# Performance work log

Hardware: AMD Instinct MI355X
Metric: run time of the kernel (lower is better)

## Reference

```python
import jax, jax.numpy as jnp
import numpy as np

N_NODES = 100000
N_EDGES = 1000000
D = 64
OUT = 64
EPS = 1e-5


def setup_inputs() -> dict:
    key = jax.random.key(0)
    k1, k2, k3, k4 = jax.random.split(key, 4)
    x = jax.random.normal(k1, (N_NODES, D), dtype=jnp.float32)
    edge_index = jax.random.randint(k2, (2, N_EDGES), 0, N_NODES, dtype=jnp.int64)
    # Linear(2*D, OUT): torch default init ~ U(-1/sqrt(fan_in), 1/sqrt(fan_in))
    bound = 1.0 / np.sqrt(2 * D)
    W = jax.random.uniform(k3, (2 * D, OUT), minval=-bound, maxval=bound, dtype=jnp.float32)
    b = jax.random.uniform(k4, (OUT,), minval=-bound, maxval=bound, dtype=jnp.float32)
    gamma = jnp.ones((OUT,), dtype=jnp.float32)
    beta = jnp.zeros((OUT,), dtype=jnp.float32)
    return {"x": x, "edge_index": edge_index, "W": W, "b": b, "gamma": gamma, "beta": beta}


def reference(x, edge_index, W, b, gamma, beta):
    row, col = edge_index[0], edge_index[1]
    # gather source features and scatter-add into destination nodes
    neighbor_sum = jax.ops.segment_sum(x[row], col, num_segments=x.shape[0])  # [N, D]
    h = jnp.concatenate([x, neighbor_sum], axis=-1)  # [N, 2D]
    h = h @ W + b  # [N, OUT]
    # LayerNorm over last dim
    mu = jnp.mean(h, axis=-1, keepdims=True)
    var = jnp.var(h, axis=-1, keepdims=True)
    h = (h - mu) * jax.lax.rsqrt(var + EPS) * gamma + beta
    return h
```

## Files before the change

### kernel.cpp

```cpp
#include <hip/hip_runtime.h>

#define NN 100000
#define NE 1000000
#define OUT_D 64
#define EPS 1e-5f

#define NB 196
#define COLS 512
#define BSTRIDE 6016
#define EPB 4096
#define NBLK1 245
#define NPROJ 1024

#define QCOLS 128
#define QCAP 2560

typedef __attribute__((ext_vector_type(8))) short bf16x8;
typedef __attribute__((ext_vector_type(4))) float f32x4;
typedef __attribute__((ext_vector_type(4))) int i32x4;

static __device__ __forceinline__ unsigned short f2bf(float f) {
    unsigned u = __float_as_uint(f);
    u += 0x7FFFu + ((u >> 16) & 1u);
    return (unsigned short)(u >> 16);
}
static __device__ __forceinline__ float bf2f(unsigned short s) {
    return __uint_as_float((unsigned)s << 16);
}

__global__ __launch_bounds__(256) void mega_kernel(
    const float* __restrict__ x, const float* __restrict__ W,
    const int* __restrict__ ei, int* __restrict__ gcur, unsigned* __restrict__ gbuf,
    unsigned short* __restrict__ y1, unsigned short* __restrict__ y2)
{
    const int tid = threadIdx.x;
    const int lane = tid & 63;
    const int wv = tid >> 6;

    if (blockIdx.x < NBLK1) {
        __shared__ int lcnt[NB];
        __shared__ int loff[NB + 1];
        __shared__ int lbase[NB];
        __shared__ int lcur[NB];
        __shared__ int wpart[4];
        __shared__ unsigned lbuf[EPB];
        __shared__ unsigned char lbkt[EPB];
        const int e0 = blockIdx.x * EPB;

        int rows[16], cols[16];
        #pragma unroll
        for (int j = 0; j < 16; ++j) {
            const int e = e0 + j * 256 + tid;
            const bool v = e < NE;
            rows[j] = v ? ei[e] : 0;
            cols[j] = v ? ei[NE + e] : -1;
        }
        for (int i = tid; i < NB; i += 256) lcnt[i] = 0;
        __syncthreads();
        #pragma unroll
        for (int j = 0; j < 16; ++j)
            if (cols[j] >= 0) atomicAdd(&lcnt[cols[j] >> 9], 1);
        __syncthreads();
        {
            const int c = (tid < NB) ? lcnt[tid] : 0;
            int s = c;
            #pragma unroll
            for (int o = 1; o < 64; o <<= 1) { int t = __shfl_up(s, o); if (lane >= o) s += t; }
            if (lane == 63) wpart[wv] = s;
            __syncthreads();
            int woff = 0;
            for (int ww = 0; ww < wv; ++ww) woff += wpart[ww];
            if (tid < NB) {
                loff[tid] = woff + s - c;
                lcur[tid] = woff + s - c;
                lbase[tid] = atomicAdd(&gcur[tid], c);
            }
            if (tid == NB - 1) loff[NB] = woff + s;
        }
        __syncthreads();
        #pragma unroll
        for (int j = 0; j < 16; ++j) {
            if (cols[j] >= 0) {
                const int b = cols[j] >> 9;
                const int p = atomicAdd(&lcur[b], 1);
                lbuf[p] = ((unsigned)rows[j] << 9) | (unsigned)(cols[j] & (COLS - 1));
                lbkt[p] = (unsigned char)b;
            }
        }
        __syncthreads();
        const int total = loff[NB];
        for (int t = tid; t < total; t += 256) {
            const int b = lbkt[t];
            const unsigned idx = (unsigned)(lbase[b] + (t - loff[b]));
            if (idx < BSTRIDE) gbuf[(size_t)b * BSTRIDE + idx] = lbuf[t];
        }
    } else {
        if (blockIdx.x == NBLK1 && tid < OUT_D)
            y2[(size_t)NN * OUT_D + tid] = 0;
        const int m = lane & 15;
        const int quad = lane >> 4;
        bf16x8 Wf[8][2];
        #pragma unroll
        for (int t = 0; t < 8; ++t)
            #pragma unroll
            for (int q = 0; q < 2; ++q) {
                bf16x8 f;
                #pragma unroll
                for (int j = 0; j < 8; ++j) {
                    const int k = q * 32 + quad * 8 + j;
                    const int krow = (t < 4) ? k : (64 + k);
                    const int col = (t & 3) * 16 + m;
                    f[j] = (short)f2bf(W[krow * 64 + col]);
                }
                Wf[t][q] = f;
            }
        for (int tile = (blockIdx.x - NBLK1) * 4 + wv; tile < NN / 16; tile += NPROJ * 4) {
            const int n0 = tile * 16;
            bf16x8 Af[2];
            #pragma unroll
            for (int q = 0; q < 2; ++q) {
                const float* px = x + (size_t)(n0 + m) * 64 + q * 32 + quad * 8;
                const f32x4 a0 = *(const f32x4*)px;
                const f32x4 a1 = *(const f32x4*)(px + 4);
                bf16x8 f;
                #pragma unroll
                for (int j = 0; j < 4; ++j) { f[j] = (short)f2bf(a0[j]); f[4 + j] = (short)f2bf(a1[j]); }
                Af[q] = f;
            }
            #pragma unroll
            for (int t = 0; t < 8; ++t) {
                f32x4 acc = {0.f, 0.f, 0.f, 0.f};
                acc = __builtin_amdgcn_mfma_f32_16x16x32_bf16(Af[0], Wf[t][0], acc, 0, 0, 0);
                acc = __builtin_amdgcn_mfma_f32_16x16x32_bf16(Af[1], Wf[t][1], acc, 0, 0, 0);
                unsigned short* __restrict__ dst = (t < 4) ? y1 : y2;
                const int colb = (t & 3) * 16 + m;
                #pragma unroll
                for (int r = 0; r < 4; ++r)
                    dst[(size_t)(n0 + quad * 4 + r) * 64 + colb] = f2bf(acc[r]);
            }
        }
    }
}

__global__ __launch_bounds__(256) void agg_kernel(
    const int* __restrict__ gcur, const unsigned* __restrict__ gbuf,
    const unsigned short* __restrict__ y1, const unsigned short* __restrict__ y2,
    const float* __restrict__ bias, const float* __restrict__ gamma,
    const float* __restrict__ beta, float* __restrict__ out)
{
    __shared__ int cofs[QCOLS + 1];
    __shared__ int ccur[QCOLS];
    __shared__ int ccnt[QCOLS];
    __shared__ int ldst[QCAP];
    const int tid = threadIdx.x;
    const int lane = tid & 63;
    const int wv = tid >> 6;
    const int b = blockIdx.x >> 2;
    const int q = blockIdx.x & 3;

    const int cntE = min(gcur[b], BSTRIDE);
    const unsigned* __restrict__ gb = gbuf + (size_t)b * BSTRIDE;

    for (int i = tid; i < QCOLS; i += 256) ccnt[i] = 0;
    for (int i = tid; i < QCAP; i += 256) ldst[i] = NN;
    __syncthreads();
    for (int i = tid; i < cntE; i += 256) {
        const unsigned p = gb[i];
        const unsigned c9 = p & 511u;
        if ((int)(c9 >> 7) == q) atomicAdd(&ccnt[c9 & (QCOLS - 1)], 1);
    }
    __syncthreads();
    if (tid < 64) {
        int v0 = (ccnt[2 * tid] + 3) & ~3;
        int v1 = (ccnt[2 * tid + 1] + 3) & ~3;
        const int tsum = v0 + v1;
        int s = tsum;
        #pragma unroll
        for (int o = 1; o < 64; o <<= 1) { int t = __shfl_up(s, o); if (tid >= o) s += t; }
        int run = s - tsum;
        cofs[2 * tid] = run;     ccur[2 * tid] = run;     run += v0;
        cofs[2 * tid + 1] = run; ccur[2 * tid + 1] = run; run += v1;
        if (tid == 63) cofs[QCOLS] = run;
    }
    __syncthreads();
    for (int i = tid; i < cntE; i += 256) {
        const unsigned p = gb[i];
        const unsigned c9 = p & 511u;
        if ((int)(c9 >> 7) == q) {
            const int pos = atomicAdd(&ccur[c9 & (QCOLS - 1)], 1);
            if (pos < QCAP) ldst[pos] = (int)(p >> 9);
        }
    }
    __syncthreads();

    const int n0 = (b << 9) + (q << 7);
    for (int cl = wv; cl < QCOLS; cl += 4) {
        const int n = n0 + cl;
        if (n >= NN) continue;
        const int st = min(cofs[cl], QCAP);
        const int en = min(cofs[cl + 1], QCAP);
        const int cnt = en - st;
        const int* __restrict__ cp = ldst + st;

        float acc = bf2f(y1[(size_t)n * OUT_D + lane]) + bias[lane];
        int i = 0;
        for (; i + 8 <= cnt; i += 8) {
            const i32x4 c0 = *(const i32x4*)(cp + i);
            const i32x4 c1 = *(const i32x4*)(cp + i + 4);
            const float v0 = bf2f(y2[(size_t)c0[0] * OUT_D + lane]);
            const float v1 = bf2f(y2[(size_t)c0[1] * OUT_D + lane]);
            const float v2 = bf2f(y2[(size_t)c0[2] * OUT_D + lane]);
            const float v3 = bf2f(y2[(size_t)c0[3] * OUT_D + lane]);
            const float v4 = bf2f(y2[(size_t)c1[0] * OUT_D + lane]);
            const float v5 = bf2f(y2[(size_t)c1[1] * OUT_D + lane]);
            const float v6 = bf2f(y2[(size_t)c1[2] * OUT_D + lane]);
            const float v7 = bf2f(y2[(size_t)c1[3] * OUT_D + lane]);
            acc += ((v0 + v1) + (v2 + v3)) + ((v4 + v5) + (v6 + v7));
        }
        if (i < cnt) {
            const i32x4 c0 = *(const i32x4*)(cp + i);
            const float v0 = bf2f(y2[(size_t)c0[0] * OUT_D + lane]);
            const float v1 = bf2f(y2[(size_t)c0[1] * OUT_D + lane]);
            const float v2 = bf2f(y2[(size_t)c0[2] * OUT_D + lane]);
            const float v3 = bf2f(y2[(size_t)c0[3] * OUT_D + lane]);
            acc += (v0 + v1) + (v2 + v3);
        }

        float sv = acc, sq = acc * acc;
        #pragma unroll
        for (int off = 32; off; off >>= 1) { sv += __shfl_xor(sv, off); sq += __shfl_xor(sq, off); }
        const float mu  = sv * (1.0f / OUT_D);
        const float var = sq * (1.0f / OUT_D) - mu * mu;
        const float inv = rsqrtf(var + EPS);
        out[(size_t)n * OUT_D + lane] = (acc - mu) * inv * gamma[lane] + beta[lane];
    }
}

extern "C" void kernel_launch(void* const* d_in, const int* in_sizes, int n_in,
                              void* d_out, int out_size, void* d_ws, size_t ws_size,
                              hipStream_t stream) {
    const float* x     = (const float*)d_in[0];
    const int*   ei    = (const int*)  d_in[1];
    const float* W     = (const float*)d_in[2];
    const float* b     = (const float*)d_in[3];
    const float* gamma = (const float*)d_in[4];
    const float* beta  = (const float*)d_in[5];
    float* out = (float*)d_out;

    char* p = (char*)d_ws;
    int*            gcur    = (int*)p;             p += 1024;
    unsigned*       gbuf    = (unsigned*)p;        p += (size_t)NB * BSTRIDE * 4;
    unsigned short* y1      = (unsigned short*)p;  p += (size_t)NN * OUT_D * 2;
    unsigned short* y2      = (unsigned short*)p;

    hipMemsetAsync(gcur, 0, NB * sizeof(int), stream);
    mega_kernel<<<NBLK1 + NPROJ, 256, 0, stream>>>(x, W, ei, gcur, gbuf, y1, y2);
    agg_kernel <<<NB * 4,        256, 0, stream>>>(gcur, gbuf, y1, y2, b, gamma, beta, out);
}
```

Measured before the change: 163.6 us.

## Interleave four destination nodes per wave in aggregation and use 512-thread blocks

Each wave in the aggregation kernel now gathers neighbor rows for four destination nodes at once, over a shared number of rounds of eight. This puts up to 32 independent y2 loads in flight per iteration, to hide gather latency better than walking one node at a time. Blocks grow to 512 threads (8 waves, 16 columns each), per-column padding is raised to multiples of 8, and the local edge buffer is enlarged to fit the extra padding. In exchange, every node in a group of four runs as many rounds as its highest-degree member, with padded slots reading a dummy row. That adds redundant loads and uses more registers per thread.

```diff
diff --git a/kernel.cpp b/kernel.cpp
--- a/kernel.cpp
+++ b/kernel.cpp
@@ -13,7 +13,7 @@
 #define NPROJ 1024
 
 #define QCOLS 128
-#define QCAP 2560
+#define QCAP 3072
 
 typedef __attribute__((ext_vector_type(8))) short bf16x8;
 typedef __attribute__((ext_vector_type(4))) float f32x4;
@@ -142,7 +142,7 @@
     }
 }
 
-__global__ __launch_bounds__(256) void agg_kernel(
+__global__ __launch_bounds__(512) void agg_kernel(
     const int* __restrict__ gcur, const unsigned* __restrict__ gbuf,
     const unsigned short* __restrict__ y1, const unsigned short* __restrict__ y2,
     const float* __restrict__ bias, const float* __restrict__ gamma,
@@ -161,18 +161,18 @@
     const int cntE = min(gcur[b], BSTRIDE);
     const unsigned* __restrict__ gb = gbuf + (size_t)b * BSTRIDE;
 
-    for (int i = tid; i < QCOLS; i += 256) ccnt[i] = 0;
-    for (int i = tid; i < QCAP; i += 256) ldst[i] = NN;
-    __syncthreads();
-    for (int i = tid; i < cntE; i += 256) {
+    for (int i = tid; i < QCOLS; i += 512) ccnt[i] = 0;
+    for (int i = tid; i < QCAP; i += 512) ldst[i] = NN;
+    __syncthreads();
+    for (int i = tid; i < cntE; i += 512) {
         const unsigned p = gb[i];
         const unsigned c9 = p & 511u;
         if ((int)(c9 >> 7) == q) atomicAdd(&ccnt[c9 & (QCOLS - 1)], 1);
     }
     __syncthreads();
     if (tid < 64) {
-        int v0 = (ccnt[2 * tid] + 3) & ~3;
-        int v1 = (ccnt[2 * tid + 1] + 3) & ~3;
+        int v0 = (ccnt[2 * tid] + 7) & ~7;
+        int v1 = (ccnt[2 * tid + 1] + 7) & ~7;
         const int tsum = v0 + v1;
         int s = tsum;
         #pragma unroll
@@ -183,7 +183,7 @@
         if (tid == 63) cofs[QCOLS] = run;
     }
     __syncthreads();
-    for (int i = tid; i < cntE; i += 256) {
+    for (int i = tid; i < cntE; i += 512) {
         const unsigned p = gb[i];
         const unsigned c9 = p & 511u;
         if ((int)(c9 >> 7) == q) {
@@ -194,45 +194,68 @@
     __syncthreads();
 
     const int n0 = (b << 9) + (q << 7);
-    for (int cl = wv; cl < QCOLS; cl += 4) {
-        const int n = n0 + cl;
-        if (n >= NN) continue;
-        const int st = min(cofs[cl], QCAP);
-        const int en = min(cofs[cl + 1], QCAP);
-        const int cnt = en - st;
-        const int* __restrict__ cp = ldst + st;
-
-        float acc = bf2f(y1[(size_t)n * OUT_D + lane]) + bias[lane];
-        int i = 0;
-        for (; i + 8 <= cnt; i += 8) {
-            const i32x4 c0 = *(const i32x4*)(cp + i);
-            const i32x4 c1 = *(const i32x4*)(cp + i + 4);
-            const float v0 = bf2f(y2[(size_t)c0[0] * OUT_D + lane]);
-            const float v1 = bf2f(y2[(size_t)c0[1] * OUT_D + lane]);
-            const float v2 = bf2f(y2[(size_t)c0[2] * OUT_D + lane]);
-            const float v3 = bf2f(y2[(size_t)c0[3] * OUT_D + lane]);
-            const float v4 = bf2f(y2[(size_t)c1[0] * OUT_D + lane]);
-            const float v5 = bf2f(y2[(size_t)c1[1] * OUT_D + lane]);
-            const float v6 = bf2f(y2[(size_t)c1[2] * OUT_D + lane]);
-            const float v7 = bf2f(y2[(size_t)c1[3] * OUT_D + lane]);
-            acc += ((v0 + v1) + (v2 + v3)) + ((v4 + v5) + (v6 + v7));
-        }
-        if (i < cnt) {
-            const i32x4 c0 = *(const i32x4*)(cp + i);
-            const float v0 = bf2f(y2[(size_t)c0[0] * OUT_D + lane]);
-            const float v1 = bf2f(y2[(size_t)c0[1] * OUT_D + lane]);
-            const float v2 = bf2f(y2[(size_t)c0[2] * OUT_D + lane]);
-            const float v3 = bf2f(y2[(size_t)c0[3] * OUT_D + lane]);
-            acc += (v0 + v1) + (v2 + v3);
-        }
-
-        float sv = acc, sq = acc * acc;
-        #pragma unroll
-        for (int off = 32; off; off >>= 1) { sv += __shfl_xor(sv, off); sq += __shfl_xor(sq, off); }
-        const float mu  = sv * (1.0f / OUT_D);
-        const float var = sq * (1.0f / OUT_D) - mu * mu;
-        const float inv = rsqrtf(var + EPS);
-        out[(size_t)n * OUT_D + lane] = (acc - mu) * inv * gamma[lane] + beta[lane];
+    #pragma unroll 1
+    for (int g = 0; g < 4; ++g) {
+        const int cl0 = wv * 16 + g * 4;
+        float acc[4];
+        int st4[4], cnt4[4];
+        #pragma unroll
+        for (int k = 0; k < 4; ++k) {
+            const int n = n0 + cl0 + k;
+            const int st = min(cofs[cl0 + k], QCAP);
+            const int en = min(cofs[cl0 + k + 1], QCAP);
+            st4[k] = st;
+            cnt4[k] = en - st;
+            acc[k] = (n < NN) ? (bf2f(y1[(size_t)n * OUT_D + lane]) + bias[lane]) : 0.f;
+        }
+        const int rounds = max(max(cnt4[0], cnt4[1]), max(cnt4[2], cnt4[3])) >> 3;
+        for (int r = 0; r < rounds; ++r) {
+            const int off = r << 3;
+            i32x4 ra[4], rb[4];
+            #pragma unroll
+            for (int k = 0; k < 4; ++k) {
+                const int po = min(st4[k] + off, QCAP - 8);
+                ra[k] = *(const i32x4*)(ldst + po);
+                rb[k] = *(const i32x4*)(ldst + po + 4);
+            }
+            #pragma unroll
+            for (int k = 0; k < 4; ++k) {
+                const bool act = off < cnt4[k];
+                #pragma unroll
+                for (int j = 0; j < 4; ++j) {
+                    ra[k][j] = act ? ra[k][j] : NN;
+                    rb[k][j] = act ? rb[k][j] : NN;
+                }
+            }
+            float v[4][8];
+            #pragma unroll
+            for (int k = 0; k < 4; ++k) {
+                v[k][0] = bf2f(y2[(size_t)ra[k][0] * OUT_D + lane]);
+                v[k][1] = bf2f(y2[(size_t)ra[k][1] * OUT_D + lane]);
+                v[k][2] = bf2f(y2[(size_t)ra[k][2] * OUT_D + lane]);
+                v[k][3] = bf2f(y2[(size_t)ra[k][3] * OUT_D + lane]);
+                v[k][4] = bf2f(y2[(size_t)rb[k][0] * OUT_D + lane]);
+                v[k][5] = bf2f(y2[(size_t)rb[k][1] * OUT_D + lane]);
+                v[k][6] = bf2f(y2[(size_t)rb[k][2] * OUT_D + lane]);
+                v[k][7] = bf2f(y2[(size_t)rb[k][3] * OUT_D + lane]);
+            }
+            #pragma unroll
+            for (int k = 0; k < 4; ++k)
+                acc[k] += ((v[k][0] + v[k][1]) + (v[k][2] + v[k][3])) +
+                          ((v[k][4] + v[k][5]) + (v[k][6] + v[k][7]));
+        }
+        #pragma unroll
+        for (int k = 0; k < 4; ++k) {
+            const int n = n0 + cl0 + k;
+            if (n >= NN) continue;
+            float sv = acc[k], sq = acc[k] * acc[k];
+            #pragma unroll
+            for (int off = 32; off; off >>= 1) { sv += __shfl_xor(sv, off); sq += __shfl_xor(sq, off); }
+            const float mu  = sv * (1.0f / OUT_D);
+            const float var = sq * (1.0f / OUT_D) - mu * mu;
+            const float inv = rsqrtf(var + EPS);
+            out[(size_t)n * OUT_D + lane] = (acc[k] - mu) * inv * gamma[lane] + beta[lane];
+        }
     }
 }
 
@@ -255,5 +278,5 @@
 
     hipMemsetAsync(gcur, 0, NB * sizeof(int), stream);
     mega_kernel<<<NBLK1 + NPROJ, 256, 0, stream>>>(x, W, ei, gcur, gbuf, y1, y2);
-    agg_kernel <<<NB * 4,        256, 0, stream>>>(gcur, gbuf, y1, y2, b, gamma, beta, out);
-}
+    agg_kernel <<<NB * 4,        512, 0, stream>>>(gcur, gbuf, y1, y2, b, gamma, beta, out);
+}
```

Measured after the change: 166.4 us. No clear change (+1.7%).

## Split aggregation into CSR placement and per-node output kernels; stage W via LDS

Applied to the files above, without the earlier changes.

The old aggregation kernel had only 784 blocks, each building a local CSR and then looping over 128 nodes. It is now split into two kernels. A place kernel writes the per-quarter CSR and a packed offset/length word per node to global memory. An out kernel then launches one wavefront per node (25000 blocks) for the gather, sum and layernorm, which gives much more parallelism to hide the latency of the random gathers. Separately, the mega kernel now converts W to bf16 into LDS once per block, transposed, instead of doing scalar global loads per fragment, and its shared memory is unioned into one buffer. The cost is an extra launch plus a global round trip for the CSR, and per-quarter capacity drops from 2560 to 2016 entries, which raises the risk of truncating high-degree buckets.

```diff
diff --git a/kernel.cpp b/kernel.cpp
--- a/kernel.cpp
+++ b/kernel.cpp
@@ -8,12 +8,15 @@
 #define NB 196
 #define COLS 512
 #define BSTRIDE 6016
+#define PBSTRIDE 8064
 #define EPB 4096
 #define NBLK1 245
 #define NPROJ 1024
 
 #define QCOLS 128
-#define QCAP 2560
+#define QCAP_PL 2016
+
+#define WSTRIDE 136
 
 typedef __attribute__((ext_vector_type(8))) short bf16x8;
 typedef __attribute__((ext_vector_type(4))) float f32x4;
@@ -33,18 +36,19 @@
     const int* __restrict__ ei, int* __restrict__ gcur, unsigned* __restrict__ gbuf,
     unsigned short* __restrict__ y1, unsigned short* __restrict__ y2)
 {
+    __shared__ __align__(16) char smem[23648];
     const int tid = threadIdx.x;
     const int lane = tid & 63;
     const int wv = tid >> 6;
 
     if (blockIdx.x < NBLK1) {
-        __shared__ int lcnt[NB];
-        __shared__ int loff[NB + 1];
-        __shared__ int lbase[NB];
-        __shared__ int lcur[NB];
-        __shared__ int wpart[4];
-        __shared__ unsigned lbuf[EPB];
-        __shared__ unsigned char lbkt[EPB];
+        int*           lcnt  = (int*)smem;
+        int*           loff  = (int*)(smem + 784);
+        int*           lbase = (int*)(smem + 1572);
+        int*           lcur  = (int*)(smem + 2356);
+        int*           wpart = (int*)(smem + 3140);
+        unsigned*      lbuf  = (unsigned*)(smem + 3156);
+        unsigned char* lbkt  = (unsigned char*)(smem + 19540);
         const int e0 = blockIdx.x * EPB;
 
         int rows[16], cols[16];
@@ -97,6 +101,12 @@
     } else {
         if (blockIdx.x == NBLK1 && tid < OUT_D)
             y2[(size_t)NN * OUT_D + tid] = 0;
+        unsigned short* wlds = (unsigned short*)smem;
+        for (int i = tid; i < 128 * 64; i += 256) {
+            const int krow = i >> 6, col = i & 63;
+            wlds[col * WSTRIDE + krow] = f2bf(W[i]);
+        }
+        __syncthreads();
         const int m = lane & 15;
         const int quad = lane >> 4;
         bf16x8 Wf[8][2];
@@ -104,15 +114,9 @@
         for (int t = 0; t < 8; ++t)
             #pragma unroll
             for (int q = 0; q < 2; ++q) {
-                bf16x8 f;
-                #pragma unroll
-                for (int j = 0; j < 8; ++j) {
-                    const int k = q * 32 + quad * 8 + j;
-                    const int krow = (t < 4) ? k : (64 + k);
-                    const int col = (t & 3) * 16 + m;
-                    f[j] = (short)f2bf(W[krow * 64 + col]);
-                }
-                Wf[t][q] = f;
+                const int krow0 = q * 32 + quad * 8 + ((t < 4) ? 0 : 64);
+                const int col = (t & 3) * 16 + m;
+                Wf[t][q] = *(const bf16x8*)(wlds + col * WSTRIDE + krow0);
             }
         for (int tile = (blockIdx.x - NBLK1) * 4 + wv; tile < NN / 16; tile += NPROJ * 4) {
             const int n0 = tile * 16;
@@ -142,19 +146,15 @@
     }
 }
 
-__global__ __launch_bounds__(256) void agg_kernel(
+__global__ __launch_bounds__(256) void place_kernel(
     const int* __restrict__ gcur, const unsigned* __restrict__ gbuf,
-    const unsigned short* __restrict__ y1, const unsigned short* __restrict__ y2,
-    const float* __restrict__ bias, const float* __restrict__ gamma,
-    const float* __restrict__ beta, float* __restrict__ out)
+    int* __restrict__ csr, unsigned* __restrict__ rowpack)
 {
     __shared__ int cofs[QCOLS + 1];
     __shared__ int ccur[QCOLS];
     __shared__ int ccnt[QCOLS];
-    __shared__ int ldst[QCAP];
+    __shared__ int ldst[QCAP_PL];
     const int tid = threadIdx.x;
-    const int lane = tid & 63;
-    const int wv = tid >> 6;
     const int b = blockIdx.x >> 2;
     const int q = blockIdx.x & 3;
 
@@ -162,7 +162,7 @@
     const unsigned* __restrict__ gb = gbuf + (size_t)b * BSTRIDE;
 
     for (int i = tid; i < QCOLS; i += 256) ccnt[i] = 0;
-    for (int i = tid; i < QCAP; i += 256) ldst[i] = NN;
+    for (int i = tid; i < QCAP_PL; i += 256) ldst[i] = NN;
     __syncthreads();
     for (int i = tid; i < cntE; i += 256) {
         const unsigned p = gb[i];
@@ -188,52 +188,67 @@
         const unsigned c9 = p & 511u;
         if ((int)(c9 >> 7) == q) {
             const int pos = atomicAdd(&ccur[c9 & (QCOLS - 1)], 1);
-            if (pos < QCAP) ldst[pos] = (int)(p >> 9);
-        }
-    }
-    __syncthreads();
-
+            if (pos < QCAP_PL) ldst[pos] = (int)(p >> 9);
+        }
+    }
+    __syncthreads();
+    const int ptotal = min(cofs[QCOLS], QCAP_PL);
+    const int base = b * PBSTRIDE + q * QCAP_PL;
+    for (int i = tid; i < ptotal; i += 256) csr[base + i] = ldst[i];
     const int n0 = (b << 9) + (q << 7);
-    for (int cl = wv; cl < QCOLS; cl += 4) {
-        const int n = n0 + cl;
+    for (int c = tid; c < QCOLS; c += 256) {
+        const int n = n0 + c;
         if (n >= NN) continue;
-        const int st = min(cofs[cl], QCAP);
-        const int en = min(cofs[cl + 1], QCAP);
-        const int cnt = en - st;
-        const int* __restrict__ cp = ldst + st;
-
-        float acc = bf2f(y1[(size_t)n * OUT_D + lane]) + bias[lane];
-        int i = 0;
-        for (; i + 8 <= cnt; i += 8) {
-            const i32x4 c0 = *(const i32x4*)(cp + i);
-            const i32x4 c1 = *(const i32x4*)(cp + i + 4);
-            const float v0 = bf2f(y2[(size_t)c0[0] * OUT_D + lane]);
-            const float v1 = bf2f(y2[(size_t)c0[1] * OUT_D + lane]);
-            const float v2 = bf2f(y2[(size_t)c0[2] * OUT_D + lane]);
-            const float v3 = bf2f(y2[(size_t)c0[3] * OUT_D + lane]);
-            const float v4 = bf2f(y2[(size_t)c1[0] * OUT_D + lane]);
-            const float v5 = bf2f(y2[(size_t)c1[1] * OUT_D + lane]);
-            const float v6 = bf2f(y2[(size_t)c1[2] * OUT_D + lane]);
-            const float v7 = bf2f(y2[(size_t)c1[3] * OUT_D + lane]);
-            acc += ((v0 + v1) + (v2 + v3)) + ((v4 + v5) + (v6 + v7));
-        }
-        if (i < cnt) {
-            const i32x4 c0 = *(const i32x4*)(cp + i);
-            const float v0 = bf2f(y2[(size_t)c0[0] * OUT_D + lane]);
-            const float v1 = bf2f(y2[(size_t)c0[1] * OUT_D + lane]);
-            const float v2 = bf2f(y2[(size_t)c0[2] * OUT_D + lane]);
-            const float v3 = bf2f(y2[(size_t)c0[3] * OUT_D + lane]);
-            acc += (v0 + v1) + (v2 + v3);
-        }
-
-        float sv = acc, sq = acc * acc;
-        #pragma unroll
-        for (int off = 32; off; off >>= 1) { sv += __shfl_xor(sv, off); sq += __shfl_xor(sq, off); }
-        const float mu  = sv * (1.0f / OUT_D);
-        const float var = sq * (1.0f / OUT_D) - mu * mu;
-        const float inv = rsqrtf(var + EPS);
-        out[(size_t)n * OUT_D + lane] = (acc - mu) * inv * gamma[lane] + beta[lane];
-    }
+        const int st = min(cofs[c], QCAP_PL);
+        const int len = min(min(cofs[c + 1], QCAP_PL) - st, 511);
+        rowpack[n] = ((unsigned)(q * QCAP_PL + st) << 9) | (unsigned)len;
+    }
+}
+
+__global__ __launch_bounds__(256) void out_kernel(
+    const unsigned* __restrict__ rowpack, const int* __restrict__ csr,
+    const unsigned short* __restrict__ y1, const unsigned short* __restrict__ y2,
+    const float* __restrict__ bias, const float* __restrict__ gamma,
+    const float* __restrict__ beta, float* __restrict__ out)
+{
+    const int lane = threadIdx.x & 63;
+    const int n = __builtin_amdgcn_readfirstlane(blockIdx.x * 4 + (threadIdx.x >> 6));
+    const unsigned pk = rowpack[n];
+    const int cnt = (int)(pk & 511);
+    const i32x4* __restrict__ cs =
+        (const i32x4*)(csr + (n >> 9) * PBSTRIDE + (int)(pk >> 9));
+
+    float acc = bf2f(y1[(size_t)n * OUT_D + lane]) + bias[lane];
+    int i = 0;
+    for (; i + 8 <= cnt; i += 8) {
+        const i32x4 c0 = cs[(i >> 2)];
+        const i32x4 c1 = cs[(i >> 2) + 1];
+        const float v0 = bf2f(y2[(size_t)c0[0] * OUT_D + lane]);
+        const float v1 = bf2f(y2[(size_t)c0[1] * OUT_D + lane]);
+        const float v2 = bf2f(y2[(size_t)c0[2] * OUT_D + lane]);
+        const float v3 = bf2f(y2[(size_t)c0[3] * OUT_D + lane]);
+        const float v4 = bf2f(y2[(size_t)c1[0] * OUT_D + lane]);
+        const float v5 = bf2f(y2[(size_t)c1[1] * OUT_D + lane]);
+        const float v6 = bf2f(y2[(size_t)c1[2] * OUT_D + lane]);
+        const float v7 = bf2f(y2[(size_t)c1[3] * OUT_D + lane]);
+        acc += ((v0 + v1) + (v2 + v3)) + ((v4 + v5) + (v6 + v7));
+    }
+    if (i < cnt) {
+        const i32x4 c0 = cs[(i >> 2)];
+        const float v0 = bf2f(y2[(size_t)c0[0] * OUT_D + lane]);
+        const float v1 = bf2f(y2[(size_t)c0[1] * OUT_D + lane]);
+        const float v2 = bf2f(y2[(size_t)c0[2] * OUT_D + lane]);
+        const float v3 = bf2f(y2[(size_t)c0[3] * OUT_D + lane]);
+        acc += (v0 + v1) + (v2 + v3);
+    }
+
+    float sv = acc, sq = acc * acc;
+    #pragma unroll
+    for (int off = 32; off; off >>= 1) { sv += __shfl_xor(sv, off); sq += __shfl_xor(sq, off); }
+    const float mu  = sv * (1.0f / OUT_D);
+    const float var = sq * (1.0f / OUT_D) - mu * mu;
+    const float inv = rsqrtf(var + EPS);
+    out[(size_t)n * OUT_D + lane] = (acc - mu) * inv * gamma[lane] + beta[lane];
 }
 
 extern "C" void kernel_launch(void* const* d_in, const int* in_sizes, int n_in,
@@ -250,10 +265,13 @@
     char* p = (char*)d_ws;
     int*            gcur    = (int*)p;             p += 1024;
     unsigned*       gbuf    = (unsigned*)p;        p += (size_t)NB * BSTRIDE * 4;
+    int*            csr     = (int*)p;             p += (size_t)NB * PBSTRIDE * 4;
+    unsigned*       rowpack = (unsigned*)p;        p += (size_t)(NB * COLS) * 4;
     unsigned short* y1      = (unsigned short*)p;  p += (size_t)NN * OUT_D * 2;
     unsigned short* y2      = (unsigned short*)p;
 
     hipMemsetAsync(gcur, 0, NB * sizeof(int), stream);
-    mega_kernel<<<NBLK1 + NPROJ, 256, 0, stream>>>(x, W, ei, gcur, gbuf, y1, y2);
-    agg_kernel <<<NB * 4,        256, 0, stream>>>(gcur, gbuf, y1, y2, b, gamma, beta, out);
-}
+    mega_kernel <<<NBLK1 + NPROJ, 256, 0, stream>>>(x, W, ei, gcur, gbuf, y1, y2);
+    place_kernel<<<NB * 4, 256, 0, stream>>>(gcur, gbuf, csr, rowpack);
+    out_kernel  <<<NN / 4, 256, 0, stream>>>(rowpack, csr, y1, y2, b, gamma, beta, out);
+}
```

New measurement: 146.1 us. -10.7%, faster.
